# Performance work log

Measured on AMD Instinct MI355X. Metric: run time of the kernel, lower is better.

Reference implementation:

```python
import jax, jax.numpy as jnp
import numpy as np

B, S, D, H, Dh = 2, 1024, 2048, 16, 128
EPS = 1e-6


def setup_inputs() -> dict:
    key = jax.random.key(0)
    ks = jax.random.split(key, 8)
    hidden_states = jax.random.normal(ks[0], (B, S, D), jnp.float32)
    def qweight(k):
        return jax.random.randint(k, (D, D), -127, 128, dtype=jnp.int32)
    wq, wk, wv, wo = qweight(ks[1]), qweight(ks[2]), qweight(ks[3]), qweight(ks[4])
    def scale(k):
        # per-output-channel dequant scale ~ O(1/(127*sqrt(D)))
        return jax.random.uniform(k, (D,), jnp.float32, 0.5, 1.5) / (127.0 * np.sqrt(D))
    wq_s, wk_s, wv_s, wo_s = scale(ks[5]), scale(ks[6]), scale(ks[7]), scale(jax.random.fold_in(key, 99))
    qn_w = jnp.ones((D,), jnp.float32)
    kn_w = jnp.ones((D,), jnp.float32)
    # RoPE tables (rotate-half convention): [S, Dh]
    pos = jnp.arange(S, dtype=jnp.float32)
    inv_freq = 1.0 / (10000.0 ** (jnp.arange(0, Dh, 2, dtype=jnp.float32) / Dh))
    freqs = pos[:, None] * inv_freq[None, :]              # [S, Dh/2]
    cos = jnp.concatenate([jnp.cos(freqs)] * 2, axis=-1)  # [S, Dh]
    sin = jnp.concatenate([jnp.sin(freqs)] * 2, axis=-1)
    lengths = jnp.array([S, 3 * S // 4], dtype=jnp.int32)
    return dict(hidden_states=hidden_states, wq_s=wq_s, wk_s=wk_s, wv_s=wv_s,
                wo_s=wo_s, qn_w=qn_w, kn_w=kn_w, cos=cos, sin=sin,
                wq=wq, wk=wk, wv=wv, wo=wo, lengths=lengths)


def _q8_linear(x, w_int, scale):
    # Q8Linear: int8 weight [out,in] dequantized by per-output-channel scale
    w = w_int.astype(jnp.float32) * scale[:, None]
    return jnp.einsum('bsd,od->bso', x, w)


def _rms_norm(x, w):
    var = jnp.mean(jnp.square(x), axis=-1, keepdims=True)
    return x * jax.lax.rsqrt(var + EPS) * w


def _apply_rope(x, cos, sin):
    # x: [B,S,D] -> per-head rotate-half RoPE -> [B,S,D]
    xh = x.reshape(B, S, H, Dh)
    x1, x2 = jnp.split(xh, 2, axis=-1)
    rot = jnp.concatenate([-x2, x1], axis=-1)
    out = xh * cos[None, :, None, :] + rot * sin[None, :, None, :]
    return out.reshape(B, S, D)


def reference(hidden_states, wq_s, wk_s, wv_s, wo_s, qn_w, kn_w, cos, sin,
              wq, wk, wv, wo, lengths):
    q = _rms_norm(_q8_linear(hidden_states, wq, wq_s), qn_w)
    k = _rms_norm(_q8_linear(hidden_states, wk, wk_s), kn_w)
    v = _q8_linear(hidden_states, wv, wv_s)
    q = _apply_rope(q, cos, sin)
    k = _apply_rope(k, cos, sin)
    # [B,S,D] -> [B,H,S,Dh]
    q = q.reshape(B, S, H, Dh).transpose(0, 2, 1, 3)
    k = k.reshape(B, S, H, Dh).transpose(0, 2, 1, 3)
    v = v.reshape(B, S, H, Dh).transpose(0, 2, 1, 3)
    # length mask -> additive bias [B,1,1,S]
    positions = jnp.arange(S)
    valid = positions[None, :] < lengths[:, None]
    bias = jnp.where(valid, 0.0, -jnp.inf).astype(jnp.float32)[:, None, None, :]
    scores = jnp.einsum('bhqd,bhkd->bhqk', q, k) / np.sqrt(Dh) + bias
    probs = jax.nn.softmax(scores, axis=-1)
    attn = jnp.einsum('bhqk,bhkd->bhqd', probs, v)
    attn = attn.transpose(0, 2, 1, 3).reshape(B, S, D)
    out = _q8_linear(attn, wo, wo_s)
    return out
```

## Files before the change

### kernel.cpp

```cpp
#include <hip/hip_runtime.h>
#include <stdint.h>

typedef __bf16 bf16;
typedef bf16 bf16x8 __attribute__((ext_vector_type(8)));
typedef bf16 bf16x4 __attribute__((ext_vector_type(4)));
typedef float f32x4 __attribute__((ext_vector_type(4)));

#define B_   2
#define S_   1024
#define D_   2048
#define H_   16
#define DH_  128
#define M_   (B_*S_)
#define EPSF 1e-6f

__device__ __forceinline__ void gload_lds16(const void* g, void* l) {
    __builtin_amdgcn_global_load_lds(
        (const __attribute__((address_space(1))) void*)g,
        (__attribute__((address_space(3))) void*)l,
        16, 0, 0);
}

struct ConvArgs {
    const void* s[4];
    bf16* d[4];
};

__global__ __launch_bounds__(256) void conv_all(ConvArgs a, int n) {
    const int z = blockIdx.y;
    const int i = (blockIdx.x * 256 + threadIdx.x) * 8;
    if (i + 8 > n) return;
    bf16x8 o;
    if (z == 0) {
        const float* src = (const float*)a.s[0];
        float4 v0 = *(const float4*)(src + i);
        float4 v1 = *(const float4*)(src + i + 4);
        o[0] = (bf16)v0.x; o[1] = (bf16)v0.y; o[2] = (bf16)v0.z; o[3] = (bf16)v0.w;
        o[4] = (bf16)v1.x; o[5] = (bf16)v1.y; o[6] = (bf16)v1.z; o[7] = (bf16)v1.w;
    } else {
        const int* src = (const int*)a.s[z];
        int4 v0 = *(const int4*)(src + i);
        int4 v1 = *(const int4*)(src + i + 4);
        o[0] = (bf16)(float)v0.x; o[1] = (bf16)(float)v0.y;
        o[2] = (bf16)(float)v0.z; o[3] = (bf16)(float)v0.w;
        o[4] = (bf16)(float)v1.x; o[5] = (bf16)(float)v1.y;
        o[6] = (bf16)(float)v1.z; o[7] = (bf16)(float)v1.w;
    }
    *(bf16x8*)(a.d[z] + i) = o;
}

struct GemmArgs {
    const bf16* W[3];
    const float* Sc[3];
    void* O[3];
    int mode[3];
    const int* wo_src;
    bf16* wo_dst;
};

__global__ __launch_bounds__(512, 2) void gemm8p(const bf16* __restrict__ A, GemmArgs args) {
    __shared__ char lds[131072];
    constexpr int NT = D_ / 64;
    const int z = blockIdx.z;
    const int t = threadIdx.x;

    if (z == 3) {
        const int flat = blockIdx.y * 8 + blockIdx.x;
        const int* src = args.wo_src + (size_t)flat * 65536;
        bf16* dst = args.wo_dst + (size_t)flat * 65536;
#pragma unroll
        for (int it = 0; it < 16; ++it) {
            int off = it * 4096 + t * 8;
            int4 v0 = *(const int4*)(src + off);
            int4 v1 = *(const int4*)(src + off + 4);
            bf16x8 o;
            o[0] = (bf16)(float)v0.x; o[1] = (bf16)(float)v0.y;
            o[2] = (bf16)(float)v0.z; o[3] = (bf16)(float)v0.w;
            o[4] = (bf16)(float)v1.x; o[5] = (bf16)(float)v1.y;
            o[6] = (bf16)(float)v1.z; o[7] = (bf16)(float)v1.w;
            *(bf16x8*)(dst + off) = o;
        }
        return;
    }

    const bf16* __restrict__ Wz = args.W[z];
    const float* __restrict__ Sc = args.Sc[z];
    const int mode = args.mode[z];
    const int w = t >> 6, l = t & 63;
    const int wr = w >> 2, wc = w & 3;
    const int fid = blockIdx.x + 8 * blockIdx.y;
    const int xcd = fid & 7, lid = fid >> 3;
    const int tx = (xcd & 1) * 4 + (lid & 3);
    const int ty = (xcd >> 1) * 2 + (lid >> 2);
    const int m0 = ty * 256, n0 = tx * 256;
    const int hi = l >> 4, lo = l & 15;

    const int r8 = l >> 3;
    const int ce = ((l & 7) ^ (r8 & 7)) * 8;
    const bf16* Ag = A  + (size_t)(m0 + w * 8 + r8) * D_ + ce;
    const bf16* Bg = Wz + (size_t)(n0 + w * 8 + r8) * D_ + ce;

    auto stage = [&](int kt, int q) {
        if (kt >= NT) return;
        const bf16* g = (q < 2 ? Ag : Bg) + (size_t)((q & 1) * 128) * D_ + (size_t)kt * 64;
        char* d = lds + ((kt & 1) ? 65536 : 0) + q * 16384 + w * 1024;
        gload_lds16((const void*)g, (void*)d);
        gload_lds16((const void*)(g + (size_t)64 * D_), (void*)(d + 8192));
    };

    f32x4 acc[8][4] = {};

    stage(0, 0); stage(0, 1); stage(0, 2); stage(0, 3);
    stage(1, 2); stage(1, 0);
    asm volatile("s_waitcnt vmcnt(4)" ::: "memory");
    asm volatile("s_barrier" ::: "memory");

    for (int kt = 0; kt < NT; ++kt) {
        const char* Pb = lds + ((kt & 1) ? 65536 : 0);
        const char* As = Pb;
        const char* Bs = Pb + 32768;
        bf16x8 a[4][2], b01[2][2], b23[2][2];

        auto rdA = [&](int mi, int kk) -> bf16x8 {
            int row = wr * 128 + mi * 16 + lo;
            return *(const bf16x8*)(As + row * 128 + ((kk * 64 + hi * 16) ^ ((row & 7) << 4)));
        };
        auto rdB = [&](int ni, int kk) -> bf16x8 {
            int row = wc * 64 + ni * 16 + lo;
            return *(const bf16x8*)(Bs + row * 128 + ((kk * 64 + hi * 16) ^ ((row & 7) << 4)));
        };

#pragma unroll
        for (int mi = 0; mi < 4; ++mi) { a[mi][0] = rdA(mi, 0); a[mi][1] = rdA(mi, 1); }
#pragma unroll
        for (int ni = 0; ni < 2; ++ni) { b01[ni][0] = rdB(ni, 0); b01[ni][1] = rdB(ni, 1); }
        stage(kt + 1, 1);
        asm volatile("s_barrier" ::: "memory");
        asm volatile("s_waitcnt lgkmcnt(0)" ::: "memory");
        __builtin_amdgcn_sched_barrier(0);
        __builtin_amdgcn_s_setprio(1);
#pragma unroll
        for (int mi = 0; mi < 4; ++mi)
#pragma unroll
            for (int ni = 0; ni < 2; ++ni)
#pragma unroll
                for (int kk = 0; kk < 2; ++kk)
                    acc[mi][ni] = __builtin_amdgcn_mfma_f32_16x16x32_bf16(a[mi][kk], b01[ni][kk], acc[mi][ni], 0, 0, 0);
        __builtin_amdgcn_s_setprio(0);
        asm volatile("s_barrier" ::: "memory");

#pragma unroll
        for (int ni = 0; ni < 2; ++ni) { b23[ni][0] = rdB(2 + ni, 0); b23[ni][1] = rdB(2 + ni, 1); }
        stage(kt + 1, 3);
        asm volatile("s_barrier" ::: "memory");
        asm volatile("s_waitcnt lgkmcnt(0)" ::: "memory");
        __builtin_amdgcn_sched_barrier(0);
        __builtin_amdgcn_s_setprio(1);
#pragma unroll
        for (int mi = 0; mi < 4; ++mi)
#pragma unroll
            for (int ni = 0; ni < 2; ++ni)
#pragma unroll
                for (int kk = 0; kk < 2; ++kk)
                    acc[mi][2 + ni] = __builtin_amdgcn_mfma_f32_16x16x32_bf16(a[mi][kk], b23[ni][kk], acc[mi][2 + ni], 0, 0, 0);
        __builtin_amdgcn_s_setprio(0);
        asm volatile("s_barrier" ::: "memory");

#pragma unroll
        for (int mi = 0; mi < 4; ++mi) { a[mi][0] = rdA(4 + mi, 0); a[mi][1] = rdA(4 + mi, 1); }
        stage(kt + 2, 2);
        asm volatile("s_barrier" ::: "memory");
        asm volatile("s_waitcnt lgkmcnt(0)" ::: "memory");
        __builtin_amdgcn_sched_barrier(0);
        __builtin_amdgcn_s_setprio(1);
#pragma unroll
        for (int mi = 0; mi < 4; ++mi)
#pragma unroll
            for (int ni = 0; ni < 2; ++ni)
#pragma unroll
                for (int kk = 0; kk < 2; ++kk)
                    acc[4 + mi][2 + ni] = __builtin_amdgcn_mfma_f32_16x16x32_bf16(a[mi][kk], b23[ni][kk], acc[4 + mi][2 + ni], 0, 0, 0);
        __builtin_amdgcn_s_setprio(0);
        asm volatile("s_barrier" ::: "memory");

        stage(kt + 2, 0);
        asm volatile("s_barrier" ::: "memory");
        __builtin_amdgcn_sched_barrier(0);
        __builtin_amdgcn_s_setprio(1);
#pragma unroll
        for (int mi = 0; mi < 4; ++mi)
#pragma unroll
            for (int ni = 0; ni < 2; ++ni)
#pragma unroll
                for (int kk = 0; kk < 2; ++kk)
                    acc[4 + mi][ni] = __builtin_amdgcn_mfma_f32_16x16x32_bf16(a[mi][kk], b01[ni][kk], acc[4 + mi][ni], 0, 0, 0);
        __builtin_amdgcn_s_setprio(0);
        if (kt < NT - 2) asm volatile("s_waitcnt vmcnt(4)" ::: "memory");
        else             asm volatile("s_waitcnt vmcnt(0)" ::: "memory");
        asm volatile("s_barrier" ::: "memory");
    }

#pragma unroll
    for (int ni = 0; ni < 4; ++ni) {
        const int n = n0 + wc * 64 + ni * 16 + lo;
        const float scv = Sc[n];
#pragma unroll
        for (int mi = 0; mi < 8; ++mi) {
            const int mb = m0 + wr * 128 + mi * 16 + hi * 4;
            if (mode == 1) {
                bf16x4 pk;
#pragma unroll
                for (int r = 0; r < 4; ++r) pk[r] = (bf16)(acc[mi][ni][r] * scv);
                const int bb = mb >> 10, s = mb & 1023, hh = n >> 7, dh = n & 127;
                *(bf16x4*)(((bf16*)args.O[z]) + (((size_t)(bb * H_ + hh)) * DH_ + dh) * S_ + s) = pk;
            } else {
#pragma unroll
                for (int r = 0; r < 4; ++r)
                    ((bf16*)args.O[z])[(size_t)(mb + r) * D_ + n] = (bf16)(acc[mi][ni][r] * scv);
            }
        }
    }
}

__global__ __launch_bounds__(256, 2) void gemmO(const bf16* __restrict__ A, const bf16* __restrict__ W,
                                                const float* __restrict__ Sc, float* __restrict__ O) {
    __shared__ char lds[65536];
    constexpr int NT = D_ / 64;
    const int t = threadIdx.x;
    const int w = t >> 6, l = t & 63;
    const int wr = w >> 1, wc = w & 1;
    const int fid = blockIdx.x + 16 * blockIdx.y;
    const int xcd = fid & 7, lid = fid >> 3;
    const int tx = (xcd & 3) * 4 + (lid & 3);
    const int ty = (xcd >> 2) * 8 + (lid >> 2);
    const int m0 = ty * 128, n0 = tx * 128;
    const int hi = l >> 4, lo = l & 15;

    const int r8 = l >> 3;
    const int ce = ((l & 7) ^ (r8 & 7)) * 8;
    const bf16* Ag = A + (size_t)(m0 + w * 8 + r8) * D_ + ce;
    const bf16* Bg = W + (size_t)(n0 + w * 8 + r8) * D_ + ce;

    auto stage = [&](int kt) {
        char* d = lds + (kt & 1) * 32768 + w * 1024;
        const bf16* ga = Ag + (size_t)kt * 64;
        const bf16* gb = Bg + (size_t)kt * 64;
#pragma unroll
        for (int j = 0; j < 4; ++j) {
            gload_lds16((const void*)(ga + (size_t)j * 32 * D_), (void*)(d + j * 4096));
            gload_lds16((const void*)(gb + (size_t)j * 32 * D_), (void*)(d + 16384 + j * 4096));
        }
    };

    f32x4 acc[4][4] = {};
    stage(0);
    for (int kt = 0; kt < NT; ++kt) {
        const char* cur = lds + (kt & 1) * 32768;
        if (kt + 1 < NT) {
            stage(kt + 1);
            asm volatile("s_waitcnt vmcnt(8)" ::: "memory");
        } else {
            asm volatile("s_waitcnt vmcnt(0)" ::: "memory");
        }
        asm volatile("s_barrier" ::: "memory");

        bf16x8 a[4][2], b[4][2];
#pragma unroll
        for (int mi = 0; mi < 4; ++mi)
#pragma unroll
            for (int kk = 0; kk < 2; ++kk) {
                int row = wr * 64 + mi * 16 + lo;
                a[mi][kk] = *(const bf16x8*)(cur + row * 128 + ((kk * 64 + hi * 16) ^ ((row & 7) << 4)));
            }
#pragma unroll
        for (int ni = 0; ni < 4; ++ni)
#pragma unroll
            for (int kk = 0; kk < 2; ++kk) {
                int row = wc * 64 + ni * 16 + lo;
                b[ni][kk] = *(const bf16x8*)(cur + 16384 + row * 128 + ((kk * 64 + hi * 16) ^ ((row & 7) << 4)));
            }
        __builtin_amdgcn_s_setprio(1);
#pragma unroll
        for (int mi = 0; mi < 4; ++mi)
#pragma unroll
            for (int ni = 0; ni < 4; ++ni)
#pragma unroll
                for (int kk = 0; kk < 2; ++kk)
                    acc[mi][ni] = __builtin_amdgcn_mfma_f32_16x16x32_bf16(a[mi][kk], b[ni][kk], acc[mi][ni], 0, 0, 0);
        __builtin_amdgcn_s_setprio(0);
        asm volatile("s_barrier" ::: "memory");
    }

#pragma unroll
    for (int ni = 0; ni < 4; ++ni) {
        const int n = n0 + wc * 64 + ni * 16 + lo;
        const float scv = Sc[n];
#pragma unroll
        for (int mi = 0; mi < 4; ++mi) {
            const int mb = m0 + wr * 64 + mi * 16 + hi * 4;
#pragma unroll
            for (int r = 0; r < 4; ++r)
                O[(size_t)(mb + r) * D_ + n] = acc[mi][ni][r] * scv;
        }
    }
}

__global__ __launch_bounds__(256) void rope_norm(const bf16* __restrict__ qr, const bf16* __restrict__ kr,
                                                 const float* __restrict__ qn, const float* __restrict__ kn,
                                                 const float* __restrict__ cosT, const float* __restrict__ sinT,
                                                 bf16* __restrict__ qOut, bf16* __restrict__ kOut) {
    const int which = blockIdx.z;
    const bf16* src = which ? kr : qr;
    const float* nw = which ? kn : qn;
    bf16* dst = which ? kOut : qOut;
    const int row = blockIdx.x;
    const int b = row >> 10, s = row & 1023;
    const int t = threadIdx.x;
    __shared__ float xs[D_];
    __shared__ float red[4];

    bf16x8 v = *(const bf16x8*)(src + (size_t)row * D_ + t * 8);
    float x[8]; float ss = 0.f;
#pragma unroll
    for (int j = 0; j < 8; ++j) { x[j] = (float)v[j]; ss += x[j] * x[j]; xs[t * 8 + j] = x[j]; }
#pragma unroll
    for (int msk = 32; msk; msk >>= 1) ss += __shfl_xor(ss, msk, 64);
    if ((t & 63) == 0) red[t >> 6] = ss;
    __syncthreads();
    const float inv = rsqrtf((red[0] + red[1] + red[2] + red[3]) / (float)D_ + EPSF);

    const int h = t >> 4;
    const int dh0 = (t & 15) * 8;
    bf16x8 o;
#pragma unroll
    for (int j = 0; j < 8; ++j) {
        int dd = dh0 + j;
        int d = h * 128 + dd;
        int pd = (dd < 64) ? d + 64 : d - 64;
        float xn = x[j] * inv * nw[d];
        float xp = xs[pd] * inv * nw[pd];
        float rot = (dd < 64) ? -xp : xp;
        o[j] = (bf16)(xn * cosT[s * DH_ + dd] + rot * sinT[s * DH_ + dd]);
    }
    *(bf16x8*)(dst + (((size_t)(b * H_ + h)) * S_ + s) * DH_ + dh0) = o;
}

__global__ __launch_bounds__(256) void flash(const bf16* __restrict__ Q, const bf16* __restrict__ Kb,
                                             const bf16* __restrict__ VTb, const int* __restrict__ lengths,
                                             bf16* __restrict__ Out) {
    __shared__ bf16 Qs[64 * 128];
    __shared__ bf16 Ks[64 * 128];
    __shared__ bf16 Vt[128 * 64];
    __shared__ bf16 Ps[4][16 * 64];
    const int t = threadIdx.x, w = t >> 6, l = t & 63;
    const int bh = blockIdx.y;
    const int b = bh >> 4;
    const int q0 = blockIdx.x * 64;
    const int L = lengths[b];
    const size_t base = (size_t)bh * S_ * DH_;
    const size_t vbase = (size_t)bh * DH_ * S_;
    const int hi = l >> 4, lo = l & 15;
    const int swz = (lo & 7) << 3;

    {
        const bf16* src = Q + base + (size_t)q0 * DH_;
#pragma unroll
        for (int i = 0; i < 4; ++i) {
            int r = (w * 4 + i) * 4 + (l >> 4);
            int sb = ((l & 15) * 16) ^ ((r & 7) << 4);
            gload_lds16((const void*)(src + (size_t)r * DH_ + (sb >> 1)), (void*)(Qs + (w * 4 + i) * 512));
        }
    }

    f32x4 O[8] = {};
    float mrow[4], lrow[4];
#pragma unroll
    for (int r = 0; r < 4; ++r) { mrow[r] = -1e30f; lrow[r] = 0.f; }
    const int nt = (L + 63) >> 6;
    const float sscale = 0.08838834764831843f;

    for (int kt = 0; kt < nt; ++kt) {
        const int k0 = kt * 64;
        __syncthreads();
        {
            const bf16* ksrc = Kb + base + (size_t)k0 * DH_;
#pragma unroll
            for (int i = 0; i < 4; ++i) {
                int r = (w * 4 + i) * 4 + (l >> 4);
                int sb = ((l & 15) * 16) ^ ((r & 7) << 4);
                gload_lds16((const void*)(ksrc + (size_t)r * DH_ + (sb >> 1)), (void*)(Ks + (w * 4 + i) * 512));
            }
        }
        {
            const bf16* vsrc = VTb + vbase + k0;
#pragma unroll
            for (int i = 0; i < 4; ++i) {
                int d = (w * 4 + i) * 8 + (l >> 3);
                int sb = ((l & 7) * 16) ^ ((d & 7) << 4);
                gload_lds16((const void*)(vsrc + (size_t)d * S_ + (sb >> 1)), (void*)(Vt + (w * 4 + i) * 512));
            }
        }
        __syncthreads();

        f32x4 sc[4] = {};
#pragma unroll
        for (int kk = 0; kk < 4; ++kk) {
            const int ko = kk * 32 + hi * 8;
            bf16x8 aq = *(const bf16x8*)(Qs + (w * 16 + lo) * 128 + (ko ^ swz));
#pragma unroll
            for (int ni = 0; ni < 4; ++ni) {
                bf16x8 bk = *(const bf16x8*)(Ks + (ni * 16 + lo) * 128 + (ko ^ swz));
                sc[ni] = __builtin_amdgcn_mfma_f32_16x16x32_bf16(aq, bk, sc[ni], 0, 0, 0);
            }
        }

        float p[4][4];
#pragma unroll
        for (int r = 0; r < 4; ++r) {
            float sv[4]; float vmax = -1e30f;
#pragma unroll
            for (int ni = 0; ni < 4; ++ni) {
                int kg = k0 + ni * 16 + lo;
                float vv = sc[ni][r] * sscale;
                if (kg >= L) vv = -1e30f;
                sv[ni] = vv;
                vmax = fmaxf(vmax, vv);
            }
#pragma unroll
            for (int msk = 1; msk < 16; msk <<= 1) vmax = fmaxf(vmax, __shfl_xor(vmax, msk, 64));
            float mnew = fmaxf(mrow[r], vmax);
            float corr = __expf(mrow[r] - mnew);
            float rs = 0.f;
#pragma unroll
            for (int ni = 0; ni < 4; ++ni) { float pv = __expf(sv[ni] - mnew); p[r][ni] = pv; rs += pv; }
#pragma unroll
            for (int msk = 1; msk < 16; msk <<= 1) rs += __shfl_xor(rs, msk, 64);
            lrow[r] = lrow[r] * corr + rs;
            mrow[r] = mnew;
#pragma unroll
            for (int di = 0; di < 8; ++di) O[di][r] *= corr;
        }

#pragma unroll
        for (int r = 0; r < 4; ++r) {
            int prow = hi * 4 + r;
#pragma unroll
            for (int ni = 0; ni < 4; ++ni)
                Ps[w][prow * 64 + (((ni * 16 + lo)) ^ ((prow & 7) << 3))] = (bf16)p[r][ni];
        }

#pragma unroll
        for (int kk = 0; kk < 2; ++kk) {
            const int ko = kk * 32 + hi * 8;
            bf16x8 ap = *(const bf16x8*)(&Ps[w][lo * 64 + (ko ^ swz)]);
#pragma unroll
            for (int di = 0; di < 8; ++di) {
                bf16x8 bv = *(const bf16x8*)(Vt + (di * 16 + lo) * 64 + (ko ^ swz));
                O[di] = __builtin_amdgcn_mfma_f32_16x16x32_bf16(ap, bv, O[di], 0, 0, 0);
            }
        }
    }

    const int h = bh & 15;
#pragma unroll
    for (int r = 0; r < 4; ++r) {
        float invl = 1.0f / lrow[r];
        int qrow = q0 + w * 16 + hi * 4 + r;
        bf16* orow = Out + (size_t)(b * S_ + qrow) * D_ + h * DH_;
#pragma unroll
        for (int di = 0; di < 8; ++di)
            orow[di * 16 + lo] = (bf16)(O[di][r] * invl);
    }
}

extern "C" void kernel_launch(void* const* d_in, const int* in_sizes, int n_in,
                              void* d_out, int out_size, void* d_ws, size_t ws_size,
                              hipStream_t stream) {
    const float* x    = (const float*)d_in[0];
    const float* wq_s = (const float*)d_in[1];
    const float* wk_s = (const float*)d_in[2];
    const float* wv_s = (const float*)d_in[3];
    const float* wo_s = (const float*)d_in[4];
    const float* qn   = (const float*)d_in[5];
    const float* kn   = (const float*)d_in[6];
    const float* cosT = (const float*)d_in[7];
    const float* sinT = (const float*)d_in[8];
    const int* wq = (const int*)d_in[9];
    const int* wk = (const int*)d_in[10];
    const int* wv = (const int*)d_in[11];
    const int* wo = (const int*)d_in[12];
    const int* lengths = (const int*)d_in[13];
    float* out = (float*)d_out;

    char* ws = (char*)d_ws;
    const size_t SLOT = (size_t)M_ * D_ * sizeof(bf16);
    bf16* xb   = (bf16*)(ws);
    bf16* wqb  = (bf16*)(ws + 1 * SLOT);
    bf16* wkb  = (bf16*)(ws + 2 * SLOT);
    bf16* wvb  = (bf16*)(ws + 3 * SLOT);
    bf16* wob  = (bf16*)(ws + 4 * SLOT);
    bf16* qr   = (bf16*)(ws + 5 * SLOT);
    bf16* kr   = (bf16*)(ws + 6 * SLOT);
    bf16* qb2  = (bf16*)(ws + 7 * SLOT);
    bf16* kb2  = (bf16*)(ws + 8 * SLOT);
    bf16* vb2  = (bf16*)(ws + 9 * SLOT);
    bf16* attnb = qr;

    const int NW = D_ * D_;
    ConvArgs ca;
    ca.s[0] = x;  ca.d[0] = xb;
    ca.s[1] = wq; ca.d[1] = wqb;
    ca.s[2] = wk; ca.d[2] = wkb;
    ca.s[3] = wv; ca.d[3] = wvb;
    conv_all<<<dim3(NW / 2048, 4), dim3(256), 0, stream>>>(ca, NW);

    GemmArgs ga;
    ga.W[0] = wqb; ga.W[1] = wkb; ga.W[2] = wvb;
    ga.Sc[0] = wq_s; ga.Sc[1] = wk_s; ga.Sc[2] = wv_s;
    ga.O[0] = qr; ga.O[1] = kr; ga.O[2] = vb2;
    ga.mode[0] = 2; ga.mode[1] = 2; ga.mode[2] = 1;
    ga.wo_src = wo; ga.wo_dst = wob;
    gemm8p<<<dim3(D_ / 256, M_ / 256, 4), dim3(512), 0, stream>>>(xb, ga);

    rope_norm<<<dim3(M_, 1, 2), dim3(256), 0, stream>>>(qr, kr, qn, kn, cosT, sinT, qb2, kb2);

    flash<<<dim3(S_ / 64, B_ * H_, 1), dim3(256), 0, stream>>>(qb2, kb2, vb2, lengths, attnb);

    gemmO<<<dim3(D_ / 128, M_ / 128), dim3(256), 0, stream>>>(attnb, wob, wo_s, out);
}
```

Baseline: 153.7 us.

## Drop XCD tile remap, merge Q/K rope-norm blocks, add lazy softmax rescale

Both GEMM kernels now map tiles straight from blockIdx instead of using the XCD-aware swizzled mapping, which may lower L2 reuse across chiplets. The rope_norm kernel handles Q and K in one block, loading the cos/sin tables once and halving the number of blocks. The flash kernel skips the running-max update and the O rescale unless the new max exceeds the old one by more than 8, which avoids exps and multiplies. The skipped rescale adds a wave-divergent branch and relies on fp32 headroom.

```diff
diff --git a/kernel.cpp b/kernel.cpp
--- a/kernel.cpp
+++ b/kernel.cpp
@@ -88,11 +88,7 @@
     const int mode = args.mode[z];
     const int w = t >> 6, l = t & 63;
     const int wr = w >> 2, wc = w & 3;
-    const int fid = blockIdx.x + 8 * blockIdx.y;
-    const int xcd = fid & 7, lid = fid >> 3;
-    const int tx = (xcd & 1) * 4 + (lid & 3);
-    const int ty = (xcd >> 1) * 2 + (lid >> 2);
-    const int m0 = ty * 256, n0 = tx * 256;
+    const int m0 = blockIdx.y * 256, n0 = blockIdx.x * 256;
     const int hi = l >> 4, lo = l & 15;
 
     const int r8 = l >> 3;
@@ -229,11 +225,7 @@
     const int t = threadIdx.x;
     const int w = t >> 6, l = t & 63;
     const int wr = w >> 1, wc = w & 1;
-    const int fid = blockIdx.x + 16 * blockIdx.y;
-    const int xcd = fid & 7, lid = fid >> 3;
-    const int tx = (xcd & 3) * 4 + (lid & 3);
-    const int ty = (xcd >> 2) * 8 + (lid >> 2);
-    const int m0 = ty * 128, n0 = tx * 128;
+    const int m0 = blockIdx.y * 128, n0 = blockIdx.x * 128;
     const int hi = l >> 4, lo = l & 15;
 
     const int r8 = l >> 3;
@@ -309,40 +301,51 @@
                                                  const float* __restrict__ qn, const float* __restrict__ kn,
                                                  const float* __restrict__ cosT, const float* __restrict__ sinT,
                                                  bf16* __restrict__ qOut, bf16* __restrict__ kOut) {
-    const int which = blockIdx.z;
-    const bf16* src = which ? kr : qr;
-    const float* nw = which ? kn : qn;
-    bf16* dst = which ? kOut : qOut;
     const int row = blockIdx.x;
     const int b = row >> 10, s = row & 1023;
     const int t = threadIdx.x;
     __shared__ float xs[D_];
     __shared__ float red[4];
 
-    bf16x8 v = *(const bf16x8*)(src + (size_t)row * D_ + t * 8);
-    float x[8]; float ss = 0.f;
-#pragma unroll
-    for (int j = 0; j < 8; ++j) { x[j] = (float)v[j]; ss += x[j] * x[j]; xs[t * 8 + j] = x[j]; }
-#pragma unroll
-    for (int msk = 32; msk; msk >>= 1) ss += __shfl_xor(ss, msk, 64);
-    if ((t & 63) == 0) red[t >> 6] = ss;
-    __syncthreads();
-    const float inv = rsqrtf((red[0] + red[1] + red[2] + red[3]) / (float)D_ + EPSF);
-
     const int h = t >> 4;
     const int dh0 = (t & 15) * 8;
-    bf16x8 o;
+    float cv[8], sv8[8];
 #pragma unroll
     for (int j = 0; j < 8; ++j) {
-        int dd = dh0 + j;
-        int d = h * 128 + dd;
-        int pd = (dd < 64) ? d + 64 : d - 64;
-        float xn = x[j] * inv * nw[d];
-        float xp = xs[pd] * inv * nw[pd];
-        float rot = (dd < 64) ? -xp : xp;
-        o[j] = (bf16)(xn * cosT[s * DH_ + dd] + rot * sinT[s * DH_ + dd]);
-    }
-    *(bf16x8*)(dst + (((size_t)(b * H_ + h)) * S_ + s) * DH_ + dh0) = o;
+        cv[j]  = cosT[s * DH_ + dh0 + j];
+        sv8[j] = sinT[s * DH_ + dh0 + j];
+    }
+
+#pragma unroll
+    for (int which = 0; which < 2; ++which) {
+        const bf16* src = which ? kr : qr;
+        const float* nw = which ? kn : qn;
+        bf16* dst = which ? kOut : qOut;
+
+        bf16x8 v = *(const bf16x8*)(src + (size_t)row * D_ + t * 8);
+        float x[8]; float ss = 0.f;
+#pragma unroll
+        for (int j = 0; j < 8; ++j) { x[j] = (float)v[j]; ss += x[j] * x[j]; xs[t * 8 + j] = x[j]; }
+#pragma unroll
+        for (int msk = 32; msk; msk >>= 1) ss += __shfl_xor(ss, msk, 64);
+        if ((t & 63) == 0) red[t >> 6] = ss;
+        __syncthreads();
+        const float inv = rsqrtf((red[0] + red[1] + red[2] + red[3]) / (float)D_ + EPSF);
+
+        bf16x8 o;
+#pragma unroll
+        for (int j = 0; j < 8; ++j) {
+            int dd = dh0 + j;
+            int d = h * 128 + dd;
+            int pd = (dd < 64) ? d + 64 : d - 64;
+            float xn = x[j] * inv * nw[d];
+            float xp = xs[pd] * inv * nw[pd];
+            float rot = (dd < 64) ? -xp : xp;
+            o[j] = (bf16)(xn * cv[j] + rot * sv8[j]);
+        }
+        *(bf16x8*)(dst + (((size_t)(b * H_ + h)) * S_ + s) * DH_ + dh0) = o;
+        if (which == 0) __syncthreads();
+    }
 }
 
 __global__ __launch_bounds__(256) void flash(const bf16* __restrict__ Q, const bf16* __restrict__ Kb,
@@ -428,8 +431,9 @@
             }
 #pragma unroll
             for (int msk = 1; msk < 16; msk <<= 1) vmax = fmaxf(vmax, __shfl_xor(vmax, msk, 64));
-            float mnew = fmaxf(mrow[r], vmax);
-            float corr = __expf(mrow[r] - mnew);
+            float mnew, corr;
+            if (vmax <= mrow[r] + 8.f) { mnew = mrow[r]; corr = 1.f; }
+            else { mnew = vmax; corr = __expf(mrow[r] - mnew); }
             float rs = 0.f;
 #pragma unroll
             for (int ni = 0; ni < 4; ++ni) { float pv = __expf(sv[ni] - mnew); p[r][ni] = pv; rs += pv; }
@@ -437,8 +441,10 @@
             for (int msk = 1; msk < 16; msk <<= 1) rs += __shfl_xor(rs, msk, 64);
             lrow[r] = lrow[r] * corr + rs;
             mrow[r] = mnew;
-#pragma unroll
-            for (int di = 0; di < 8; ++di) O[di][r] *= corr;
+            if (corr != 1.f) {
+#pragma unroll
+                for (int di = 0; di < 8; ++di) O[di][r] *= corr;
+            }
         }
 
 #pragma unroll
@@ -522,7 +528,7 @@
     ga.wo_src = wo; ga.wo_dst = wob;
     gemm8p<<<dim3(D_ / 256, M_ / 256, 4), dim3(512), 0, stream>>>(xb, ga);
 
-    rope_norm<<<dim3(M_, 1, 2), dim3(256), 0, stream>>>(qr, kr, qn, kn, cosT, sinT, qb2, kb2);
+    rope_norm<<<dim3(M_), dim3(256), 0, stream>>>(qr, kr, qn, kn, cosT, sinT, qb2, kb2);
 
     flash<<<dim3(S_ / 64, B_ * H_, 1), dim3(256), 0, stream>>>(qb2, kb2, vb2, lengths, attnb);
 
```

Result: slower. 162.5 us (+5.8%).
